# Performance work log

Hardware: AMD Instinct MI355X
Metric: run time of the kernel (lower is better)

Reference implementation:

```python
import jax, jax.numpy as jnp
import numpy as np
import math

# ---- constants lifted verbatim from the torch source ----
PMLX = 10; PX = 400; TX = PMLX + PX + PMLX          # txsize = 420
PMLY = 10; PY = 400; TY = PMLY + PY + PMLY          # tysize = 420
CX = TX // 2; CY = TY // 2
EPS0 = 1e-9 / 36 / math.pi
MU0 = 4 * math.pi * 1e-7
C0 = 1.0 / math.sqrt(MU0 * EPS0)
DX = 2.5e-8; DY = 2.5e-8
DT = 0.99 / C0 / math.sqrt((1.0 / DX) ** 2 + (1.0 / DY) ** 2)
EPSR_INF = 5.283
EPS_INF = EPS0 * EPSR_INF
F0 = 5.47e14; BW = 0.1 * F0
T = math.sqrt(2.0) * math.sqrt(math.log(2.0)) / (math.pi * BW)
NSTEPS = 200   # reduced from 16000 for the correctness baseline; same per-step math


def setup_inputs() -> dict:
    # Lorentz (complex-pole) silver model from param(): pole/residue -> a0,a1,b0,b1,b2
    pr, pi_ = -4.8113e12, 6.8512e13
    rr, ri = 4.9581e14, -1.511e18
    a0 = -2.0 * (pr * rr + pi_ * ri)
    a1 = 2.0 * rr
    b0 = pr * pr + pi_ * pi_
    b1 = -2.0 * pr
    b2 = 1.0
    den = b0 * DT * DT + 2 * b1 * DT + 4 * b2
    Ca = np.array([-(2 * b0 * DT * DT - 8 * b2) / den], np.float32)
    Cb = np.array([-(b0 * DT * DT - 2 * b1 * DT + 4 * b2) / den], np.float32)
    Cc = np.array([(2 * a0 * EPS0 * DT + 4 * a1 * EPS0) / den], np.float32)
    Cd = np.array([-(8 * a1 * EPS0) / den], np.float32)
    Ce = np.array([(-2 * a0 * EPS0 * DT + 4 * a1 * EPS0) / den], np.float32)
    temp1 = float(Cc[0])                       # sum over tot_pol = 1 pole
    denom = EPS_INF / DT + 0.5 * temp1
    C1 = np.full((TX + 1, TY + 1), (EPS_INF / DT) / denom, np.float32)
    C2 = np.full((TX + 1, TY + 1), 0.5 / denom, np.float32)
    Cb_dx = np.full((TX + 1, TY + 1), 1.0 / denom / DX, np.float32)
    Cb_dy = np.full((TX + 1, TY + 1), 1.0 / denom / DY, np.float32)
    dbhx = np.full((TX + 1, TY), DT / MU0 / DY, np.float32)   # Hx curl coeff
    dbhy = np.full((TX, TY + 1), DT / MU0 / DX, np.float32)   # Hy curl coeff
    # polynomial-graded PML conductivity profiles (pml_param)
    m = 4
    eta0 = 120.0 * math.pi
    smax = 0.8 * (m + 1) / (eta0 * DX)

    def prof(n, npml, off):
        k = np.arange(n, dtype=np.float64)
        dl = np.clip(npml - k - off, 0.0, None) / npml   # depth into left PML
        dr = np.clip(k + off - (n - 1 - npml), 0.0, None) / npml
        return (smax * (dl ** m + dr ** m)).astype(np.float32)

    sig_ex = prof(TX + 1, PMLX, 0.0)
    sig_ey = prof(TY + 1, PMLY, 0.0)
    sig_hx = prof(TX, PMLX, 0.5)   # H nodes on half-grid
    sig_hy = prof(TY, PMLY, 0.5)
    # Gaussian-modulated sine soft source at the grid center
    t = np.arange(NSTEPS, dtype=np.float64) * DT
    src = (np.exp(-(((t - 4 * T) / T) ** 2)) * np.sin(2 * math.pi * F0 * (t - 4 * T))).astype(np.float32)
    return {
        "src": jnp.asarray(src), "C1": jnp.asarray(C1), "C2": jnp.asarray(C2),
        "Cb_dx": jnp.asarray(Cb_dx), "Cb_dy": jnp.asarray(Cb_dy),
        "dbhx": jnp.asarray(dbhx), "dbhy": jnp.asarray(dbhy),
        "Ca": jnp.asarray(Ca), "Cb": jnp.asarray(Cb), "Cc": jnp.asarray(Cc),
        "Cd": jnp.asarray(Cd), "Ce": jnp.asarray(Ce),
        "sig_ex": jnp.asarray(sig_ex), "sig_ey": jnp.asarray(sig_ey),
        "sig_hx": jnp.asarray(sig_hx), "sig_hy": jnp.asarray(sig_hy),
        "n_steps": NSTEPS,
    }


def reference(src, C1, C2, Cb_dx, Cb_dy, dbhx, dbhy, Ca, Cb, Cc, Cd, Ce,
              sig_ex, sig_ey, sig_hx, sig_hy, n_steps):
    # PML damping factors (exponential time-stepping of the conductive loss)
    de = jnp.exp(-(sig_ex[:, None] + sig_ey[None, :]) * (DT / EPS0))     # (421,421) for Ez
    dhx = jnp.exp(-(sig_ex[:, None] + sig_hy[None, :]) * (DT / MU0))     # (421,420) for Hx
    dhy = jnp.exp(-(sig_hx[:, None] + sig_ey[None, :]) * (DT / MU0))     # (420,421) for Hy
    # PEC outer boundary mask
    mask = jnp.pad(jnp.ones((TX - 1, TY - 1), de.dtype), ((1, 1), (1, 1)))
    ca = Ca[:, None, None]; cb = Cb[:, None, None]; cc = Cc[:, None, None]
    cd = Cd[:, None, None]; ce = Ce[:, None, None]

    def step(carry, s):
        Ez, Eold, Hx, Hy, Jz, Jold = carry
        # H-field Yee updates with PML damping
        Hx = dhx * (Hx - dbhx * (Ez[:, 1:] - Ez[:, :-1]))
        Hy = dhy * (Hy + dbhy * (Ez[1:, :] - Ez[:-1, :]))
        # curls onto Ez nodes (interior), zero-padded at PEC boundary
        curlHy = jnp.pad(Hy[1:, :] - Hy[:-1, :], ((1, 1), (0, 0)))       # (421,421)
        curlHx = jnp.pad(Hx[:, 1:] - Hx[:, :-1], ((0, 0), (1, 1)))       # (421,421)
        # Lorentz ADE dispersion source term (tot_pol summed; Cc*Ez^{n+1} folded into C1/C2/Cb_*)
        Phi = jnp.sum((ca + 1.0) * Jz + cb * Jold + cd * Ez[None] + ce * Eold[None], axis=0)
        Ez_new = mask * de * (C1 * Ez + Cb_dx * curlHy - Cb_dy * curlHx - C2 * Phi)
        Ez_new = Ez_new.at[CX, CY].add(s)                                 # soft point source
        # polarization current recurrence
        Jz_new = ca * Jz + cb * Jold + cc * Ez_new[None] + cd * Ez[None] + ce * Eold[None]
        return (Ez_new, Ez, Hx, Hy, Jz_new, Jz), None

    z = jnp.zeros((TX + 1, TY + 1), src.dtype)
    init = (z, z,
            jnp.zeros((TX + 1, TY), src.dtype),
            jnp.zeros((TX, TY + 1), src.dtype),
            jnp.zeros((1, TX + 1, TY + 1), src.dtype),
            jnp.zeros((1, TX + 1, TY + 1), src.dtype))
    (Ez, _, _, _, _, _), _ = jax.lax.scan(step, init, src[:n_steps])
    return Ez
```

## Files before the change

### kernel.cpp

```cpp
#include <hip/hip_runtime.h>
#include <math.h>

#define NXr 421
#define CXr 210
#define NSTEPS_C 200

#define Bt   16
#define Kt   8
#define EXT  32
#define SPITCH 34
#define NBLK 27
#define NPHASE (NSTEPS_C / Kt)

#define PP   448
#define PAD  8
#define CP   (CXr + PAD)
#define FSZ  (PP * PP)

struct PParams {
    float *aEz, *aEo, *aJz, *aJo, *aHx, *aHy;
    float *bEz, *bEo, *bJz, *bJo, *bHx, *bHy;
    const float *dexP, *deyP, *aexP, *aeyP, *ahxP, *ahyP;
    const float *C1a, *C2a, *Cbdxa, *Cbdya;
    const float *Caa, *Cba, *Cca, *Cda, *Cea, *dbhxa, *dbhya;
    const float *src;
};

__global__ void init_kernel(const float* __restrict__ sig_ex,
                            const float* __restrict__ sig_ey,
                            const float* __restrict__ sig_hx,
                            const float* __restrict__ sig_hy,
                            float de_fac, float dh_fac,
                            float* __restrict__ zero_base, int n_zero,
                            float* __restrict__ dexP, float* __restrict__ deyP,
                            float* __restrict__ aexP, float* __restrict__ aeyP,
                            float* __restrict__ ahxP, float* __restrict__ ahyP)
{
    int t = blockIdx.x * blockDim.x + threadIdx.x;
    int stride = gridDim.x * blockDim.x;
    for (int k = t; k < n_zero; k += stride) zero_base[k] = 0.0f;
    if (t < PP) {
        int g = t - PAD;
        dexP[t] = (g >= 1 && g <= NXr - 2) ? expf(-sig_ex[g] * de_fac) : 0.0f;
        deyP[t] = (g >= 1 && g <= NXr - 2) ? expf(-sig_ey[g] * de_fac) : 0.0f;
        aexP[t] = (g >= 0 && g <  NXr)     ? expf(-sig_ex[g] * dh_fac) : 0.0f;
        aeyP[t] = (g >= 0 && g <  NXr)     ? expf(-sig_ey[g] * dh_fac) : 0.0f;
        ahxP[t] = (g >= 0 && g <  NXr - 1) ? expf(-sig_hx[g] * dh_fac) : 0.0f;
        ahyP[t] = (g >= 0 && g <  NXr - 1) ? expf(-sig_hy[g] * dh_fac) : 0.0f;
    }
}

__global__ __launch_bounds__(256)
void phase_kernel(PParams p, int t, int b0, float* __restrict__ out,
                  int writeOut)
{
    __shared__ __align__(16) float sEz[2][EXT][SPITCH];

    const int tid = threadIdx.x;
    const int tj = tid & 15, ti = tid >> 4;
    const int li0 = 2 * ti, lj0 = 2 * tj;
    const int r0 = ((int)blockIdx.x + b0) * Bt + li0;
    const int c0 = ((int)blockIdx.y + b0) * Bt + lj0;

    const float ca = p.Caa[0], cb = p.Cba[0], cc = p.Cca[0];
    const float cd = p.Cda[0], ce = p.Cea[0];
    const float ca1 = ca + 1.0f;
    const float C1 = p.C1a[0], C2 = p.C2a[0];
    const float cbdx = p.Cbdxa[0], cbdy = p.Cbdya[0];
    const float dbhx0 = p.dbhxa[0], dbhy0 = p.dbhya[0];

    float dHx[2][2], dHy[2][2], dE[2][2], dHyU[2], dHxL[2];
    bool isSrc[2][2];
#pragma unroll
    for (int a = 0; a < 2; ++a)
#pragma unroll
        for (int b = 0; b < 2; ++b) {
            dHx[a][b] = p.aexP[r0 + a] * p.ahyP[c0 + b];
            dHy[a][b] = p.ahxP[r0 + a] * p.aeyP[c0 + b];
            dE[a][b]  = p.dexP[r0 + a] * p.deyP[c0 + b];
            isSrc[a][b] = (r0 + a == CP) && (c0 + b == CP);
        }
    {
        float ahxU = (r0 > 0) ? p.ahxP[r0 - 1] : 0.0f;
        float ahyL = (c0 > 0) ? p.ahyP[c0 - 1] : 0.0f;
        dHyU[0] = ahxU * p.aeyP[c0];
        dHyU[1] = ahxU * p.aeyP[c0 + 1];
        dHxL[0] = p.aexP[r0] * ahyL;
        dHxL[1] = p.aexP[r0 + 1] * ahyL;
    }

    const bool odd = (t & 1) != 0;
    const float* cEz = odd ? p.bEz : p.aEz;
    const float* cEo = odd ? p.bEo : p.aEo;
    const float* cJz = odd ? p.bJz : p.aJz;
    const float* cJo = odd ? p.bJo : p.aJo;
    const float* cHx = odd ? p.bHx : p.aHx;
    const float* cHy = odd ? p.bHy : p.aHy;
    float* nEz = odd ? p.aEz : p.bEz;
    float* nEo = odd ? p.aEo : p.bEo;
    float* nJz = odd ? p.aJz : p.bJz;
    float* nJo = odd ? p.aJo : p.bJo;
    float* nHx = odd ? p.aHx : p.bHx;
    float* nHy = odd ? p.aHy : p.bHy;

    float ez[2][2], eo[2][2], jz[2][2], jo[2][2], hx[2][2], hy[2][2];
#pragma unroll
    for (int a = 0; a < 2; ++a) {
        int g = (r0 + a) * PP + c0;
        float2 v;
        v = *(const float2*)&cEz[g]; ez[a][0] = v.x; ez[a][1] = v.y;
        v = *(const float2*)&cEo[g]; eo[a][0] = v.x; eo[a][1] = v.y;
        v = *(const float2*)&cJz[g]; jz[a][0] = v.x; jz[a][1] = v.y;
        v = *(const float2*)&cJo[g]; jo[a][0] = v.x; jo[a][1] = v.y;
        v = *(const float2*)&cHx[g]; hx[a][0] = v.x; hx[a][1] = v.y;
        v = *(const float2*)&cHy[g]; hy[a][0] = v.x; hy[a][1] = v.y;
    }
    float hyU[2], hxL[2];
    {
        float2 v = *(const float2*)&cHy[(r0 - 1) * PP + c0];
        hyU[0] = v.x; hyU[1] = v.y;
        hxL[0] = cHx[r0 * PP + c0 - 1];
        hxL[1] = cHx[(r0 + 1) * PP + c0 - 1];
    }

    const bool edgeR = (tj == 15), edgeD = (ti == 15);
    const bool edgeU = (ti == 0),  edgeL = (tj == 0);
    const int n0 = t * Kt;

    for (int s = 0; s < Kt; ++s) {
        float (*S)[SPITCH] = sEz[s & 1];
        *(float2*)&S[li0][lj0]     = make_float2(ez[0][0], ez[0][1]);
        *(float2*)&S[li0 + 1][lj0] = make_float2(ez[1][0], ez[1][1]);
        __syncthreads();

        float eR0 = edgeR ? 0.0f : S[li0][lj0 + 2];
        float eR1 = edgeR ? 0.0f : S[li0 + 1][lj0 + 2];
        float2 eD  = edgeD ? make_float2(0.0f, 0.0f)
                           : *(float2*)&S[li0 + 2][lj0];
        float2 eU  = edgeU ? make_float2(0.0f, 0.0f)
                           : *(float2*)&S[li0 - 1][lj0];
        float eL0 = edgeL ? 0.0f : S[li0][lj0 - 1];
        float eL1 = edgeL ? 0.0f : S[li0 + 1][lj0 - 1];

        hx[0][0] = dHx[0][0] * (hx[0][0] - dbhx0 * (ez[0][1] - ez[0][0]));
        hx[0][1] = dHx[0][1] * (hx[0][1] - dbhx0 * (eR0     - ez[0][1]));
        hx[1][0] = dHx[1][0] * (hx[1][0] - dbhx0 * (ez[1][1] - ez[1][0]));
        hx[1][1] = dHx[1][1] * (hx[1][1] - dbhx0 * (eR1     - ez[1][1]));

        hy[0][0] = dHy[0][0] * (hy[0][0] + dbhy0 * (ez[1][0] - ez[0][0]));
        hy[0][1] = dHy[0][1] * (hy[0][1] + dbhy0 * (ez[1][1] - ez[0][1]));
        hy[1][0] = dHy[1][0] * (hy[1][0] + dbhy0 * (eD.x     - ez[1][0]));
        hy[1][1] = dHy[1][1] * (hy[1][1] + dbhy0 * (eD.y     - ez[1][1]));

        hyU[0] = dHyU[0] * (hyU[0] + dbhy0 * (ez[0][0] - eU.x));
        hyU[1] = dHyU[1] * (hyU[1] + dbhy0 * (ez[0][1] - eU.y));
        hxL[0] = dHxL[0] * (hxL[0] - dbhx0 * (ez[0][0] - eL0));
        hxL[1] = dHxL[1] * (hxL[1] - dbhx0 * (ez[1][0] - eL1));

        float sv = p.src[n0 + s];
        float cHyv[2][2], cHxv[2][2];
        cHyv[0][0] = hy[0][0] - hyU[0];   cHxv[0][0] = hx[0][0] - hxL[0];
        cHyv[0][1] = hy[0][1] - hyU[1];   cHxv[0][1] = hx[0][1] - hx[0][0];
        cHyv[1][0] = hy[1][0] - hy[0][0]; cHxv[1][0] = hx[1][0] - hxL[1];
        cHyv[1][1] = hy[1][1] - hy[0][1]; cHxv[1][1] = hx[1][1] - hx[1][0];

#pragma unroll
        for (int a = 0; a < 2; ++a)
#pragma unroll
            for (int b = 0; b < 2; ++b) {
                float e = ez[a][b], eold = eo[a][b];
                float j = jz[a][b], jold = jo[a][b];
                float phi = ca1 * j + cb * jold + cd * e + ce * eold;
                float en = dE[a][b] *
                    (C1 * e + cbdx * cHyv[a][b] - cbdy * cHxv[a][b] - C2 * phi);
                if (isSrc[a][b]) en += sv;
                float jn = phi - j + cc * en;
                eo[a][b] = e;  ez[a][b] = en;
                jo[a][b] = j;  jz[a][b] = jn;
            }
    }

    if (ti >= 4 && ti < 12 && tj >= 4 && tj < 12) {
#pragma unroll
        for (int a = 0; a < 2; ++a) {
            int g = (r0 + a) * PP + c0;
            *(float2*)&nEz[g] = make_float2(ez[a][0], ez[a][1]);
            *(float2*)&nEo[g] = make_float2(eo[a][0], eo[a][1]);
            *(float2*)&nJz[g] = make_float2(jz[a][0], jz[a][1]);
            *(float2*)&nJo[g] = make_float2(jo[a][0], jo[a][1]);
            *(float2*)&nHx[g] = make_float2(hx[a][0], hx[a][1]);
            *(float2*)&nHy[g] = make_float2(hy[a][0], hy[a][1]);
        }
        if (writeOut) {
#pragma unroll
            for (int a = 0; a < 2; ++a)
#pragma unroll
                for (int b = 0; b < 2; ++b) {
                    int gi = r0 + a - PAD, gj = c0 + b - PAD;
                    if (gi < NXr && gj < NXr)
                        out[gi * NXr + gj] = ez[a][b];
                }
        }
    }
}

extern "C" void kernel_launch(void* const* d_in, const int* in_sizes, int n_in,
                              void* d_out, int out_size, void* d_ws, size_t ws_size,
                              hipStream_t stream)
{
    const float* src    = (const float*)d_in[0];
    const float* C1     = (const float*)d_in[1];
    const float* C2     = (const float*)d_in[2];
    const float* Cb_dx  = (const float*)d_in[3];
    const float* Cb_dy  = (const float*)d_in[4];
    const float* dbhx   = (const float*)d_in[5];
    const float* dbhy   = (const float*)d_in[6];
    const float* Ca     = (const float*)d_in[7];
    const float* Cb     = (const float*)d_in[8];
    const float* Cc     = (const float*)d_in[9];
    const float* Cd     = (const float*)d_in[10];
    const float* Ce     = (const float*)d_in[11];
    const float* sig_ex = (const float*)d_in[12];
    const float* sig_ey = (const float*)d_in[13];
    const float* sig_hx = (const float*)d_in[14];
    const float* sig_hy = (const float*)d_in[15];

    const double EPS0 = 1e-9 / 36.0 / M_PI;
    const double MU0  = 4.0 * M_PI * 1e-7;
    const double C0   = 1.0 / sqrt(MU0 * EPS0);
    const double DXd  = 2.5e-8, DYd = 2.5e-8;
    const double DT   = 0.99 / C0 / sqrt(1.0 / (DXd * DXd) + 1.0 / (DYd * DYd));
    const float de_fac = (float)(DT / EPS0);
    const float dh_fac = (float)(DT / MU0);

    float* base = (float*)d_ws;
    float* fields = base + PP;
    float* w = fields + 12 * (size_t)FSZ;
    float* dexP = w; w += PP;
    float* deyP = w; w += PP;
    float* aexP = w; w += PP;
    float* aeyP = w; w += PP;
    float* ahxP = w; w += PP;
    float* ahyP = w; w += PP;

    PParams p;
    p.aEz = fields + 0 * (size_t)FSZ;  p.aEo = fields + 1 * (size_t)FSZ;
    p.aJz = fields + 2 * (size_t)FSZ;  p.aJo = fields + 3 * (size_t)FSZ;
    p.aHx = fields + 4 * (size_t)FSZ;  p.aHy = fields + 5 * (size_t)FSZ;
    p.bEz = fields + 6 * (size_t)FSZ;  p.bEo = fields + 7 * (size_t)FSZ;
    p.bJz = fields + 8 * (size_t)FSZ;  p.bJo = fields + 9 * (size_t)FSZ;
    p.bHx = fields + 10 * (size_t)FSZ; p.bHy = fields + 11 * (size_t)FSZ;
    p.dexP = dexP; p.deyP = deyP; p.aexP = aexP; p.aeyP = aeyP;
    p.ahxP = ahxP; p.ahyP = ahyP;
    p.C1a = C1; p.C2a = C2; p.Cbdxa = Cb_dx; p.Cbdya = Cb_dy;
    p.Caa = Ca; p.Cba = Cb; p.Cca = Cc; p.Cda = Cd; p.Cea = Ce;
    p.dbhxa = dbhx; p.dbhya = dbhy;
    p.src = src;

    init_kernel<<<512, 256, 0, stream>>>(sig_ex, sig_ey, sig_hx, sig_hy,
                                         de_fac, dh_fac,
                                         base, PP + 12 * FSZ,
                                         dexP, deyP, aexP, aeyP, ahxP, ahyP);

    dim3 blk(256);
    for (int t = 0; t < NPHASE; ++t) {
        int R  = 8 * t + 11;
        int lo = CP - R, hi = CP + R;
        int b0 = (lo - (EXT - 1)) / 16; if (b0 < 0) b0 = 0;
        int b1 = hi / 16;               if (b1 > NBLK - 1) b1 = NBLK - 1;
        dim3 g(b1 - b0 + 1, b1 - b0 + 1);
        phase_kernel<<<g, blk, 0, stream>>>(p, t, b0, (float*)d_out,
                                            (t == NPHASE - 1) ? 1 : 0);
    }
}
```

Baseline: 282.3 us.

## Remap workgroups across XCDs and use zero-padded halo LDS tile

Measured after the change: 256.6 us. 1.1x faster.

```diff
diff --git a/kernel.cpp b/kernel.cpp
--- a/kernel.cpp
+++ b/kernel.cpp
@@ -8,7 +8,8 @@
 #define Bt   16
 #define Kt   8
 #define EXT  32
-#define SPITCH 34
+#define LROWS (EXT + 2)
+#define SPITCH 36
 #define NBLK 27
 #define NPHASE (NSTEPS_C / Kt)
 
@@ -54,13 +55,22 @@
 void phase_kernel(PParams p, int t, int b0, float* __restrict__ out,
                   int writeOut)
 {
-    __shared__ __align__(16) float sEz[2][EXT][SPITCH];
+    __shared__ __align__(16) float sEz[2][LROWS][SPITCH];
 
     const int tid = threadIdx.x;
     const int tj = tid & 15, ti = tid >> 4;
     const int li0 = 2 * ti, lj0 = 2 * tj;
-    const int r0 = ((int)blockIdx.x + b0) * Bt + li0;
-    const int c0 = ((int)blockIdx.y + b0) * Bt + lj0;
+
+    const int gx = (int)gridDim.x;
+    int orig = (int)blockIdx.y * gx + (int)blockIdx.x;
+    int nwg = gx * gx;
+    int q = nwg >> 3, rr = nwg & 7;
+    int xcd = orig & 7, k = orig >> 3;
+    int nid = (xcd < rr ? xcd * (q + 1) : rr * (q + 1) + (xcd - rr) * q) + k;
+    int bx = nid % gx, by = nid / gx;
+
+    const int r0 = (bx + b0) * Bt + li0;
+    const int c0 = (by + b0) * Bt + lj0;
 
     const float ca = p.Caa[0], cb = p.Cba[0], cc = p.Cca[0];
     const float cd = p.Cda[0], ce = p.Cea[0];
@@ -70,7 +80,7 @@
     const float dbhx0 = p.dbhxa[0], dbhy0 = p.dbhya[0];
 
     float dHx[2][2], dHy[2][2], dE[2][2], dHyU[2], dHxL[2];
-    bool isSrc[2][2];
+    float srcw[2][2];
 #pragma unroll
     for (int a = 0; a < 2; ++a)
 #pragma unroll
@@ -78,7 +88,7 @@
             dHx[a][b] = p.aexP[r0 + a] * p.ahyP[c0 + b];
             dHy[a][b] = p.ahxP[r0 + a] * p.aeyP[c0 + b];
             dE[a][b]  = p.dexP[r0 + a] * p.deyP[c0 + b];
-            isSrc[a][b] = (r0 + a == CP) && (c0 + b == CP);
+            srcw[a][b] = ((r0 + a == CP) && (c0 + b == CP)) ? 1.0f : 0.0f;
         }
     {
         float ahxU = (r0 > 0) ? p.ahxP[r0 - 1] : 0.0f;
@@ -103,6 +113,11 @@
     float* nHx = odd ? p.aHx : p.bHx;
     float* nHy = odd ? p.aHy : p.bHy;
 
+    {
+        float* sp = &sEz[0][0][0];
+        for (int z = tid; z < 2 * LROWS * SPITCH; z += 256) sp[z] = 0.0f;
+    }
+
     float ez[2][2], eo[2][2], jz[2][2], jo[2][2], hx[2][2], hy[2][2];
 #pragma unroll
     for (int a = 0; a < 2; ++a) {
@@ -123,41 +138,43 @@
         hxL[1] = cHx[(r0 + 1) * PP + c0 - 1];
     }
 
-    const bool edgeR = (tj == 15), edgeD = (ti == 15);
-    const bool edgeU = (ti == 0),  edgeL = (tj == 0);
     const int n0 = t * Kt;
+    float svl[Kt];
+#pragma unroll
+    for (int s = 0; s < Kt; ++s) svl[s] = p.src[n0 + s];
+
+    __syncthreads();
 
     for (int s = 0; s < Kt; ++s) {
         float (*S)[SPITCH] = sEz[s & 1];
-        *(float2*)&S[li0][lj0]     = make_float2(ez[0][0], ez[0][1]);
-        *(float2*)&S[li0 + 1][lj0] = make_float2(ez[1][0], ez[1][1]);
-        __syncthreads();
-
-        float eR0 = edgeR ? 0.0f : S[li0][lj0 + 2];
-        float eR1 = edgeR ? 0.0f : S[li0 + 1][lj0 + 2];
-        float2 eD  = edgeD ? make_float2(0.0f, 0.0f)
-                           : *(float2*)&S[li0 + 2][lj0];
-        float2 eU  = edgeU ? make_float2(0.0f, 0.0f)
-                           : *(float2*)&S[li0 - 1][lj0];
-        float eL0 = edgeL ? 0.0f : S[li0][lj0 - 1];
-        float eL1 = edgeL ? 0.0f : S[li0 + 1][lj0 - 1];
+        *(float2*)&S[1 + li0][2 + lj0] = make_float2(ez[0][0], ez[0][1]);
+        *(float2*)&S[2 + li0][2 + lj0] = make_float2(ez[1][0], ez[1][1]);
 
         hx[0][0] = dHx[0][0] * (hx[0][0] - dbhx0 * (ez[0][1] - ez[0][0]));
-        hx[0][1] = dHx[0][1] * (hx[0][1] - dbhx0 * (eR0     - ez[0][1]));
         hx[1][0] = dHx[1][0] * (hx[1][0] - dbhx0 * (ez[1][1] - ez[1][0]));
-        hx[1][1] = dHx[1][1] * (hx[1][1] - dbhx0 * (eR1     - ez[1][1]));
-
         hy[0][0] = dHy[0][0] * (hy[0][0] + dbhy0 * (ez[1][0] - ez[0][0]));
         hy[0][1] = dHy[0][1] * (hy[0][1] + dbhy0 * (ez[1][1] - ez[0][1]));
-        hy[1][0] = dHy[1][0] * (hy[1][0] + dbhy0 * (eD.x     - ez[1][0]));
-        hy[1][1] = dHy[1][1] * (hy[1][1] + dbhy0 * (eD.y     - ez[1][1]));
+
+        __syncthreads();
+
+        float eR0 = S[1 + li0][4 + lj0];
+        float eR1 = S[2 + li0][4 + lj0];
+        float2 eD = *(float2*)&S[3 + li0][2 + lj0];
+        float2 eU = *(float2*)&S[li0][2 + lj0];
+        float eL0 = S[1 + li0][1 + lj0];
+        float eL1 = S[2 + li0][1 + lj0];
+
+        hx[0][1] = dHx[0][1] * (hx[0][1] - dbhx0 * (eR0 - ez[0][1]));
+        hx[1][1] = dHx[1][1] * (hx[1][1] - dbhx0 * (eR1 - ez[1][1]));
+        hy[1][0] = dHy[1][0] * (hy[1][0] + dbhy0 * (eD.x - ez[1][0]));
+        hy[1][1] = dHy[1][1] * (hy[1][1] + dbhy0 * (eD.y - ez[1][1]));
 
         hyU[0] = dHyU[0] * (hyU[0] + dbhy0 * (ez[0][0] - eU.x));
         hyU[1] = dHyU[1] * (hyU[1] + dbhy0 * (ez[0][1] - eU.y));
         hxL[0] = dHxL[0] * (hxL[0] - dbhx0 * (ez[0][0] - eL0));
         hxL[1] = dHxL[1] * (hxL[1] - dbhx0 * (ez[1][0] - eL1));
 
-        float sv = p.src[n0 + s];
+        float sv = svl[s];
         float cHyv[2][2], cHxv[2][2];
         cHyv[0][0] = hy[0][0] - hyU[0];   cHxv[0][0] = hx[0][0] - hxL[0];
         cHyv[0][1] = hy[0][1] - hyU[1];   cHxv[0][1] = hx[0][1] - hx[0][0];
@@ -173,7 +190,7 @@
                 float phi = ca1 * j + cb * jold + cd * e + ce * eold;
                 float en = dE[a][b] *
                     (C1 * e + cbdx * cHyv[a][b] - cbdy * cHxv[a][b] - C2 * phi);
-                if (isSrc[a][b]) en += sv;
+                en = fmaf(srcw[a][b], sv, en);
                 float jn = phi - j + cc * en;
                 eo[a][b] = e;  ez[a][b] = en;
                 jo[a][b] = j;  jz[a][b] = jn;
```
